# Kernel optimization log

Measured on AMD Instinct MI355X. Metric: run time of the kernel, lower is better.

## Reference

```python
import jax, jax.numpy as jnp
import numpy as np

B, T, IDIM, HDIM, CDIM = 8, 2048, 512, 2048, 64
ENERGY_TH = 256


def setup_inputs() -> dict:
    key = jax.random.key(0)
    k1, k2, k3, k4, k5 = jax.random.split(key, 5)
    x = jax.random.normal(k1, (B, T, IDIM), dtype=jnp.float32)
    theta = jax.random.randint(k2, (B, T), 0, 1024, dtype=jnp.int32)
    W_enc = jax.random.normal(k3, (IDIM, HDIM), dtype=jnp.float32) * 0.02
    b_enc = jnp.zeros((HDIM,), dtype=jnp.float32)
    W_dec = jax.random.normal(k4, (HDIM, IDIM), dtype=jnp.float32) * 0.02
    b_dec = jnp.zeros((IDIM,), dtype=jnp.float32)
    return {"x": x, "theta": theta, "W_enc": W_enc, "b_enc": b_enc,
            "W_dec": W_dec, "b_dec": b_dec}


def _relay_mask(h, theta):
    # h: [B,T,HDIM], theta: [B,T] int
    energy = h * h
    _, idx = jax.lax.top_k(energy, CDIM)              # [B,T,CDIM]
    move = jnp.abs(theta - IDIM + 1) > ENERGY_TH      # [B,T] bool
    cum = jnp.cumsum(move.astype(jnp.int32), axis=-1)  # cum_move_indices
    # positions of True (in time order) come first; stable sort preserves order
    order = jnp.argsort(jnp.where(move, 0, 1), axis=-1, stable=True)  # [B,T]
    # torch: cat([ind[0:1], ind[move]])[cum]  ==>
    #   cum==0 -> timestep 0's topk indices; cum==k>0 -> k-th moved timestep's indices
    src_t = jnp.where(cum == 0, 0,
                      jnp.take_along_axis(order, jnp.maximum(cum - 1, 0), axis=-1))  # [B,T]
    b_ix = jnp.arange(B)[:, None]
    gathered = idx[b_ix, src_t]                        # [B,T,CDIM]
    t_ix = jnp.arange(T)[None, :, None]
    mask = jnp.zeros((B, T, HDIM), dtype=h.dtype).at[
        b_ix[:, :, None] * jnp.ones_like(gathered), t_ix, gathered].set(1.0)
    return mask


def reference(x, theta, W_enc, b_enc, W_dec, b_dec):
    # encoder_type='linear', mask_prev=None (first hsr call), decoder='self'
    h = jnp.einsum('bti,ih->bth', x, W_enc) + b_enc   # [B,T,HDIM]
    mask = _relay_mask(h, theta)                       # mask_cur == mask_prev out
    h = h * mask                                       # masked_fill(~mask, 0)
    out = jnp.einsum('bth,hi->bti', h, W_dec) + b_dec  # [B,T,IDIM]
    return out, mask
```

## Files before the change

kernel.cpp:

```cpp
#include <hip/hip_runtime.h>


typedef _Float16 f16x8 __attribute__((ext_vector_type(8)));
typedef _Float16 f16x4 __attribute__((ext_vector_type(4)));
typedef float    f32x4 __attribute__((ext_vector_type(4)));
typedef unsigned int uint;
typedef unsigned short ushort;

constexpr int Mrows = 16384;
constexpr int Kdim  = 512;
constexpr int Ndim  = 2048;

__device__ __forceinline__ void gl16(const void* g, void* l) {
    __builtin_amdgcn_global_load_lds(
        (const __attribute__((address_space(1))) void*)g,
        (__attribute__((address_space(3))) void*)l, 16, 0, 0);
}

__global__ __launch_bounds__(256) void split_x_kernel(
    const float* __restrict__ x, _Float16* __restrict__ xh, _Float16* __restrict__ xl) {
    int i = blockIdx.x * 256 + threadIdx.x;
    float4 v = ((const float4*)x)[i];
    f16x4 h, l;
    float vv[4] = {v.x, v.y, v.z, v.w};
#pragma unroll
    for (int j = 0; j < 4; ++j) {
        _Float16 hj = (_Float16)vv[j];
        h[j] = hj;
        l[j] = (_Float16)((vv[j] - (float)hj) * 2048.0f);
    }
    *(f16x4*)(xh + i * 4) = h;
    *(f16x4*)(xl + i * 4) = l;
}

__global__ __launch_bounds__(256) void split_w_kernel(
    const float* __restrict__ W, _Float16* __restrict__ Wh, _Float16* __restrict__ Wl) {
    __shared__ float T[32][33];
    int n0 = blockIdx.x * 32, k0 = blockIdx.y * 32;
    int tid = threadIdx.x;
    int c = tid & 31, r0 = tid >> 5;
#pragma unroll
    for (int i = 0; i < 4; ++i) {
        int r = r0 + 8 * i;
        T[r][c] = W[(size_t)(k0 + r) * Ndim + n0 + c];
    }
    __syncthreads();
#pragma unroll
    for (int i = 0; i < 4; ++i) {
        int r = r0 + 8 * i;
        float ws = T[c][r] * 1024.0f;
        _Float16 wh = (_Float16)ws;
        _Float16 wl = (_Float16)((ws - (float)wh) * 2048.0f);
        size_t o = (size_t)(n0 + r) * Kdim + k0 + c;
        Wh[o] = wh;
        Wl[o] = wl;
    }
}

__global__ __launch_bounds__(256) void gemm_split_kernel(
    const _Float16* __restrict__ Xh, const _Float16* __restrict__ Xl,
    const _Float16* __restrict__ Wh, const _Float16* __restrict__ Wl,
    const float* __restrict__ benc, float* __restrict__ H) {
    __shared__ _Float16 Ah[8 * 512], Al[8 * 512];
    __shared__ _Float16 Bh[8 * 512], Bl[8 * 512];
    int tid = threadIdx.x;
    int bn = blockIdx.x, bm = blockIdx.y;
    int wave = tid >> 6, lane = tid & 63;
    int wm = wave >> 1, wn = wave & 1;

    f32x4 accP[4][4] = {};
    f32x4 accQ[4][4] = {};

    int f0 = wave * 2;
    int lrow = f0 * 16 + (lane & 15);
    int lcol = (lane >> 4) * 8;
    const _Float16* gA_h = Xh + ((size_t)(bm * 128) + lrow) * Kdim + lcol;
    const _Float16* gA_l = Xl + ((size_t)(bm * 128) + lrow) * Kdim + lcol;
    const _Float16* gB_h = Wh + ((size_t)(bn * 128) + lrow) * Kdim + lcol;
    const _Float16* gB_l = Wl + ((size_t)(bn * 128) + lrow) * Kdim + lcol;
    _Float16* lA_h = &Ah[f0 * 512];
    _Float16* lA_l = &Al[f0 * 512];
    _Float16* lB_h = &Bh[f0 * 512];
    _Float16* lB_l = &Bl[f0 * 512];
    constexpr int FSTRIDE = 16 * 512;

    for (int k0 = 0; k0 < Kdim; k0 += 32) {
        gl16(gA_h + k0, lA_h);  gl16(gA_h + k0 + FSTRIDE, lA_h + 512);
        gl16(gA_l + k0, lA_l);  gl16(gA_l + k0 + FSTRIDE, lA_l + 512);
        gl16(gB_h + k0, lB_h);  gl16(gB_h + k0 + FSTRIDE, lB_h + 512);
        gl16(gB_l + k0, lB_l);  gl16(gB_l + k0 + FSTRIDE, lB_l + 512);
        __syncthreads();

        f16x8 ah[4], al8[4], bh8[4], bl8[4];
#pragma unroll
        for (int mf = 0; mf < 4; ++mf) {
            int off = (wm * 4 + mf) * 512 + lane * 8;
            ah[mf]  = *(const f16x8*)&Ah[off];
            al8[mf] = *(const f16x8*)&Al[off];
        }
#pragma unroll
        for (int nf = 0; nf < 4; ++nf) {
            int off = (wn * 4 + nf) * 512 + lane * 8;
            bh8[nf] = *(const f16x8*)&Bh[off];
            bl8[nf] = *(const f16x8*)&Bl[off];
        }
#pragma unroll
        for (int mf = 0; mf < 4; ++mf)
#pragma unroll
            for (int nf = 0; nf < 4; ++nf) {
                accP[mf][nf] = __builtin_amdgcn_mfma_f32_16x16x32_f16(
                    ah[mf], bh8[nf], accP[mf][nf], 0, 0, 0);
                accQ[mf][nf] = __builtin_amdgcn_mfma_f32_16x16x32_f16(
                    ah[mf], bl8[nf], accQ[mf][nf], 0, 0, 0);
                accQ[mf][nf] = __builtin_amdgcn_mfma_f32_16x16x32_f16(
                    al8[mf], bh8[nf], accQ[mf][nf], 0, 0, 0);
            }
        __syncthreads();
    }

    int rsub = (lane >> 4) * 4;
#pragma unroll
    for (int nf = 0; nf < 4; ++nf) {
        int col = bn * 128 + wn * 64 + nf * 16 + (lane & 15);
        float bias = benc[col];
#pragma unroll
        for (int mf = 0; mf < 4; ++mf) {
            int rowb = bm * 128 + wm * 64 + mf * 16 + rsub;
#pragma unroll
            for (int r = 0; r < 4; ++r)
                H[(size_t)(rowb + r) * Ndim + col] =
                    (accP[mf][nf][r] + accQ[mf][nf][r] * (1.0f / 2048.0f)) * (1.0f / 1024.0f) + bias;
        }
    }
}

__global__ __launch_bounds__(256) void topk_kernel(
    const float* __restrict__ H, int* __restrict__ IDX) {
    int row = blockIdx.x, tid = threadIdx.x;
    __shared__ uint keys[2048];
    __shared__ uint hist[2048];
    __shared__ uint csum[256];
    __shared__ uint cand[2048];
    __shared__ uint s_pivbin, s_r, s_n, s_nc;
    const float* hrow = H + (size_t)row * Ndim;

    int base = tid * 8;
#pragma unroll
    for (int j = 0; j < 8; j += 4) {
        float4 v = *(const float4*)(hrow + base + j);
        keys[base + j]     = __float_as_uint(v.x * v.x);
        keys[base + j + 1] = __float_as_uint(v.y * v.y);
        keys[base + j + 2] = __float_as_uint(v.z * v.z);
        keys[base + j + 3] = __float_as_uint(v.w * v.w);
        *(uint4*)&hist[base + j] = make_uint4(0, 0, 0, 0);
    }
    if (tid == 0) { s_n = 0; s_nc = 0; }
    __syncthreads();
#pragma unroll
    for (int j = 0; j < 8; ++j)
        atomicAdd(&hist[keys[base + j] >> 21], 1u);
    __syncthreads();
    uint c = 0;
#pragma unroll
    for (int j = 0; j < 8; ++j) c += hist[base + j];
    csum[tid] = c;
    __syncthreads();
    for (int off = 1; off < 256; off <<= 1) {
        uint v = (tid + off < 256) ? csum[tid + off] : 0;
        __syncthreads();
        csum[tid] += v;
        __syncthreads();
    }
    uint above = (tid < 255) ? csum[tid + 1] : 0;
    if (csum[tid] >= 64 && above < 64) {
        uint cge = above;
        for (int b = 8 * tid + 7; b >= 8 * tid; --b) {
            cge += hist[b];
            if (cge >= 64) { s_pivbin = (uint)b; s_r = 64 - (cge - hist[b]); break; }
        }
    }
    __syncthreads();
    uint P = s_pivbin, r = s_r;
    int* o = IDX + (size_t)row * 64;
#pragma unroll
    for (int j = 0; j < 8; ++j) {
        uint k = keys[base + j];
        uint bin = k >> 21;
        if (bin > P) {
            o[atomicAdd(&s_n, 1u)] = base + j;
        } else if (bin == P) {
            cand[atomicAdd(&s_nc, 1u)] = ((k & 0x1FFFFFu) << 11) | (2047u - (uint)(base + j));
        }
    }
    __syncthreads();
    uint nc = s_nc;
    for (uint ci = tid; ci < nc; ci += 256) {
        uint me = cand[ci];
        uint rank = 0;
        for (uint j = 0; j < nc; ++j) rank += (cand[j] > me);
        if (rank < r) {
            o[atomicAdd(&s_n, 1u)] = 2047 - (int)(me & 0x7FFu);
        }
    }
}

__global__ __launch_bounds__(256) void srct_kernel(
    const int* __restrict__ theta, int* __restrict__ srct) {
    __shared__ int cmax[256];
    int b = blockIdx.x, tid = threadIdx.x;
    const int* th = theta + b * 2048;
    int loc[8];
    int run = -1;
    int base = tid * 8;
#pragma unroll
    for (int j = 0; j < 8; ++j) {
        int d = th[base + j] - 511; d = d < 0 ? -d : d;
        if (d > 256) run = base + j;
        loc[j] = run;
    }
    cmax[tid] = run;
    __syncthreads();
    for (int off = 1; off < 256; off <<= 1) {
        int v = (tid >= off) ? cmax[tid - off] : -1;
        __syncthreads();
        if (v > cmax[tid]) cmax[tid] = v;
        __syncthreads();
    }
    int exc = (tid == 0) ? -1 : cmax[tid - 1];
    int* o = srct + b * 2048;
#pragma unroll
    for (int j = 0; j < 8; ++j) {
        int v = loc[j] > exc ? loc[j] : exc;
        o[base + j] = v < 0 ? 0 : v;
    }
}

__global__ __launch_bounds__(256) void out_kernel(
    float* Hm, const int* __restrict__ IDX, const int* __restrict__ SRCT,
    const float* __restrict__ Wd, const float* __restrict__ bd,
    float* __restrict__ outp) {
    int row = blockIdx.x, tid = threadIdx.x;
    int b = row >> 11;
    __shared__ int c[64];
    __shared__ float hv[64];
    __shared__ float mrow[2048];
    int s = SRCT[row];
    if (tid < 64) c[tid] = IDX[((size_t)((b << 11) + s)) * 64 + tid];
    float4 z = {0.f, 0.f, 0.f, 0.f};
    *(float4*)&mrow[tid * 8] = z;
    *(float4*)&mrow[tid * 8 + 4] = z;
    __syncthreads();
    if (tid < 64) {
        int ci = c[tid];
        hv[tid] = Hm[(size_t)row * Ndim + ci];
        mrow[ci] = 1.0f;
    }
    __syncthreads();
    int i0 = tid * 2;
    float a0 = bd[i0], a1 = bd[i0 + 1];
#pragma unroll 8
    for (int j = 0; j < 64; ++j) {
        float h = hv[j];
        float2 w = *(const float2*)(Wd + (size_t)c[j] * Kdim + i0);
        a0 += h * w.x;
        a1 += h * w.y;
    }
    *(float2*)(outp + (size_t)row * Kdim + i0) = make_float2(a0, a1);
    *(float4*)(Hm + (size_t)row * Ndim + tid * 8)     = *(float4*)&mrow[tid * 8];
    *(float4*)(Hm + (size_t)row * Ndim + tid * 8 + 4) = *(float4*)&mrow[tid * 8 + 4];
}

extern "C" void kernel_launch(void* const* d_in, const int* in_sizes, int n_in,
                              void* d_out, int out_size, void* d_ws, size_t ws_size,
                              hipStream_t stream) {
    const float* X  = (const float*)d_in[0];
    const int*   TH = (const int*)d_in[1];
    const float* WE = (const float*)d_in[2];
    const float* BE = (const float*)d_in[3];
    const float* WD = (const float*)d_in[4];
    const float* BD = (const float*)d_in[5];

    float* OUT = (float*)d_out;
    float* H   = OUT + (size_t)Mrows * Kdim;

    _Float16* Xh = (_Float16*)OUT;
    _Float16* Xl = Xh + (size_t)Mrows * Kdim;

    char* ws = (char*)d_ws;
    _Float16* Wh  = (_Float16*)ws;
    _Float16* Wl  = (_Float16*)(ws + 2097152u);
    int*      IDX = (int*)(ws + 4194304u);
    int*      SRCT= (int*)(ws + 8388608u);

    split_x_kernel<<<8192, 256, 0, stream>>>(X, Xh, Xl);
    split_w_kernel<<<dim3(64, 16), 256, 0, stream>>>(WE, Wh, Wl);
    gemm_split_kernel<<<dim3(Ndim / 128, Mrows / 128), 256, 0, stream>>>(
        Xh, Xl, Wh, Wl, BE, H);
    topk_kernel<<<Mrows, 256, 0, stream>>>(H, IDX);
    srct_kernel<<<8, 256, 0, stream>>>(TH, SRCT);
    out_kernel<<<Mrows, 256, 0, stream>>>(H, IDX, SRCT, WD, BD, OUT);
}
```

Measured before the change: 633.9 us.

## Double-buffer LDS tiles in split GEMM and remap workgroups across XCDs

Turns the encoder GEMM's K loop into a double-buffered pipeline. The next K-slice is loaded straight into LDS while MFMAs run on the current buffer, and one barrier per iteration replaces two. The grid also becomes 1D, with a block-id remap that gives each of the 8 XCDs a contiguous run of tiles to improve L2 reuse of the shared A and B panels. LDS use doubles to 64KB per block, which may reduce occupancy. Correctness also depends on the async loads completing by the barrier.

```diff
diff --git a/kernel.cpp b/kernel.cpp
--- a/kernel.cpp
+++ b/kernel.cpp
@@ -61,10 +61,13 @@
     const _Float16* __restrict__ Xh, const _Float16* __restrict__ Xl,
     const _Float16* __restrict__ Wh, const _Float16* __restrict__ Wl,
     const float* __restrict__ benc, float* __restrict__ H) {
-    __shared__ _Float16 Ah[8 * 512], Al[8 * 512];
-    __shared__ _Float16 Bh[8 * 512], Bl[8 * 512];
+    __shared__ _Float16 Ah[2][8 * 512], Al[2][8 * 512];
+    __shared__ _Float16 Bh[2][8 * 512], Bl[2][8 * 512];
     int tid = threadIdx.x;
-    int bn = blockIdx.x, bm = blockIdx.y;
+    int orig = blockIdx.x;
+    int wgid = (orig & 7) * 256 + (orig >> 3);
+    int bn = wgid & 15;
+    int bm = wgid >> 4;
     int wave = tid >> 6, lane = tid & 63;
     int wm = wave >> 1, wn = wave & 1;
 
@@ -78,45 +81,60 @@
     const _Float16* gA_l = Xl + ((size_t)(bm * 128) + lrow) * Kdim + lcol;
     const _Float16* gB_h = Wh + ((size_t)(bn * 128) + lrow) * Kdim + lcol;
     const _Float16* gB_l = Wl + ((size_t)(bn * 128) + lrow) * Kdim + lcol;
-    _Float16* lA_h = &Ah[f0 * 512];
-    _Float16* lA_l = &Al[f0 * 512];
-    _Float16* lB_h = &Bh[f0 * 512];
-    _Float16* lB_l = &Bl[f0 * 512];
     constexpr int FSTRIDE = 16 * 512;
-
-    for (int k0 = 0; k0 < Kdim; k0 += 32) {
-        gl16(gA_h + k0, lA_h);  gl16(gA_h + k0 + FSTRIDE, lA_h + 512);
-        gl16(gA_l + k0, lA_l);  gl16(gA_l + k0 + FSTRIDE, lA_l + 512);
-        gl16(gB_h + k0, lB_h);  gl16(gB_h + k0 + FSTRIDE, lB_h + 512);
-        gl16(gB_l + k0, lB_l);  gl16(gB_l + k0 + FSTRIDE, lB_l + 512);
-        __syncthreads();
-
-        f16x8 ah[4], al8[4], bh8[4], bl8[4];
-#pragma unroll
-        for (int mf = 0; mf < 4; ++mf) {
-            int off = (wm * 4 + mf) * 512 + lane * 8;
-            ah[mf]  = *(const f16x8*)&Ah[off];
-            al8[mf] = *(const f16x8*)&Al[off];
-        }
-#pragma unroll
-        for (int nf = 0; nf < 4; ++nf) {
-            int off = (wn * 4 + nf) * 512 + lane * 8;
-            bh8[nf] = *(const f16x8*)&Bh[off];
-            bl8[nf] = *(const f16x8*)&Bl[off];
-        }
-#pragma unroll
-        for (int mf = 0; mf < 4; ++mf)
-#pragma unroll
-            for (int nf = 0; nf < 4; ++nf) {
-                accP[mf][nf] = __builtin_amdgcn_mfma_f32_16x16x32_f16(
-                    ah[mf], bh8[nf], accP[mf][nf], 0, 0, 0);
-                accQ[mf][nf] = __builtin_amdgcn_mfma_f32_16x16x32_f16(
-                    ah[mf], bl8[nf], accQ[mf][nf], 0, 0, 0);
-                accQ[mf][nf] = __builtin_amdgcn_mfma_f32_16x16x32_f16(
-                    al8[mf], bh8[nf], accQ[mf][nf], 0, 0, 0);
-            }
-        __syncthreads();
-    }
+    int ldst = f0 * 512;
+
+#define STAGE(buf, kof)                                                     \
+    do {                                                                    \
+        gl16(gA_h + (kof), &Ah[buf][ldst]);                                 \
+        gl16(gA_h + (kof) + FSTRIDE, &Ah[buf][ldst + 512]);                 \
+        gl16(gA_l + (kof), &Al[buf][ldst]);                                 \
+        gl16(gA_l + (kof) + FSTRIDE, &Al[buf][ldst + 512]);                 \
+        gl16(gB_h + (kof), &Bh[buf][ldst]);                                 \
+        gl16(gB_h + (kof) + FSTRIDE, &Bh[buf][ldst + 512]);                 \
+        gl16(gB_l + (kof), &Bl[buf][ldst]);                                 \
+        gl16(gB_l + (kof) + FSTRIDE, &Bl[buf][ldst + 512]);                 \
+    } while (0)
+
+#define COMPUTE(buf)                                                        \
+    do {                                                                    \
+        f16x8 ah[4], al8[4], bh8[4], bl8[4];                                \
+        _Pragma("unroll")                                                   \
+        for (int mf = 0; mf < 4; ++mf) {                                    \
+            int off = (wm * 4 + mf) * 512 + lane * 8;                       \
+            ah[mf]  = *(const f16x8*)&Ah[buf][off];                         \
+            al8[mf] = *(const f16x8*)&Al[buf][off];                         \
+        }                                                                   \
+        _Pragma("unroll")                                                   \
+        for (int nf = 0; nf < 4; ++nf) {                                    \
+            int off = (wn * 4 + nf) * 512 + lane * 8;                       \
+            bh8[nf] = *(const f16x8*)&Bh[buf][off];                         \
+            bl8[nf] = *(const f16x8*)&Bl[buf][off];                         \
+        }                                                                   \
+        _Pragma("unroll")                                                   \
+        for (int mf = 0; mf < 4; ++mf)                                      \
+            _Pragma("unroll")                                               \
+            for (int nf = 0; nf < 4; ++nf) {                                \
+                accP[mf][nf] = __builtin_amdgcn_mfma_f32_16x16x32_f16(      \
+                    ah[mf], bh8[nf], accP[mf][nf], 0, 0, 0);                \
+                accQ[mf][nf] = __builtin_amdgcn_mfma_f32_16x16x32_f16(      \
+                    ah[mf], bl8[nf], accQ[mf][nf], 0, 0, 0);                \
+                accQ[mf][nf] = __builtin_amdgcn_mfma_f32_16x16x32_f16(      \
+                    al8[mf], bh8[nf], accQ[mf][nf], 0, 0, 0);               \
+            }                                                               \
+    } while (0)
+
+    STAGE(0, 0);
+    __syncthreads();
+    int cur = 0;
+#pragma unroll 1
+    for (int t = 0; t < 15; ++t) {
+        STAGE(cur ^ 1, (t + 1) * 32);
+        COMPUTE(cur);
+        __syncthreads();
+        cur ^= 1;
+    }
+    COMPUTE(cur);
 
     int rsub = (lane >> 4) * 4;
 #pragma unroll
@@ -132,6 +150,8 @@
                     (accP[mf][nf][r] + accQ[mf][nf][r] * (1.0f / 2048.0f)) * (1.0f / 1024.0f) + bias;
         }
     }
+#undef STAGE
+#undef COMPUTE
 }
 
 __global__ __launch_bounds__(256) void topk_kernel(
@@ -294,8 +314,7 @@
 
     split_x_kernel<<<8192, 256, 0, stream>>>(X, Xh, Xl);
     split_w_kernel<<<dim3(64, 16), 256, 0, stream>>>(WE, Wh, Wl);
-    gemm_split_kernel<<<dim3(Ndim / 128, Mrows / 128), 256, 0, stream>>>(
-        Xh, Xl, Wh, Wl, BE, H);
+    gemm_split_kernel<<<2048, 256, 0, stream>>>(Xh, Xl, Wh, Wl, BE, H);
     topk_kernel<<<Mrows, 256, 0, stream>>>(H, IDX);
     srct_kernel<<<8, 256, 0, stream>>>(TH, SRCT);
     out_kernel<<<Mrows, 256, 0, stream>>>(H, IDX, SRCT, WD, BD, OUT);
```

New measurement: 536.4 us. 15.4% less time.
